# Optimization experiments

Hardware: AMD Instinct MI355X
Metric: run time of the kernel (lower is better)

The kernel has to match this reference:

```python
import jax, jax.numpy as jnp
import numpy as np

DELTA_PULL = 0.5
DELTA_PUSH = 1.5
EPS = 1e-6


def setup_inputs() -> dict:
    key = jax.random.key(0)
    k1, k2 = jax.random.split(key)
    B, C, H, W, K = 4, 16, 512, 512, 16
    embedding_maps = jax.random.normal(k1, (B, C, H, W), dtype=jnp.float32)
    instance_masks = jax.random.randint(k2, (B, K, H, W), 0, 2, dtype=jnp.int32)
    return {"embedding_maps": embedding_maps, "instance_masks": instance_masks}


def reference(embedding_maps, instance_masks):
    emb = embedding_maps                      # [B, C, H, W]
    m = (instance_masks > 0).astype(emb.dtype)  # [B, K, H, W]
    K = m.shape[1]

    # per-instance masked segment reductions over all H*W pixels
    counts = m.sum((-1, -2))                                   # [B, K]
    sums = jnp.einsum('bchw,bkhw->bkc', emb, m)                # [B, K, C]
    sq_sums = jnp.einsum('bchw,bkhw->bkc', emb * emb, m)       # [B, K, C]

    valid = counts > 0                                          # [B, K]
    safe_counts = jnp.maximum(counts, 1.0)
    means = sums / safe_counts[..., None]                       # [B, K, C] exact fg mean

    # sum over fg pixels of ||e - mean||^2 = sq_sum - 2*mean.sum + n*mean^2
    pull_k = (sq_sums - 2.0 * means * sums + counts[..., None] * means * means).sum(-1)
    pull_k = jnp.where(valid, pull_k / (counts + EPS), 0.0)     # [B, K]

    M = valid.sum(-1).astype(emb.dtype)                         # [B] num valid instances
    pull_b = pull_k.sum(-1) / jnp.maximum(M, 1.0)               # [B]

    # pairwise push between valid instance means (i < j)
    diff = means[:, :, None, :] - means[:, None, :, :]          # [B, K, K, C]
    dist = jnp.sqrt((diff * diff).sum(-1) + 1e-12)              # [B, K, K]
    iu = jnp.arange(K)
    pair = valid[:, :, None] & valid[:, None, :] & (iu[:, None] < iu[None, :])
    push_terms = jnp.where(pair, jnp.maximum(DELTA_PUSH - dist, 0.0) ** 2, 0.0)
    npairs = M * (M - 1.0) / 2.0
    push_b = jnp.where(M > 1.0, push_terms.sum((-1, -2)) / jnp.maximum(npairs, 1.0), 0.0)

    return (DELTA_PULL * pull_b + push_b).mean()
```

## Files before the change

kernel.cpp:

```cpp
#include <hip/hip_runtime.h>

#define BB 4
#define CC 16
#define KK 16
#define HWP (512 * 512)
#define TPB 1024
#define TPW 256
#define NTILES (HWP / TPB)
#define THREADS 256
#define NGROUP (TPW / 32)
#define NSLICE 16
#define WSTOT (64 + 1024 + 1024)

typedef short bf16x8 __attribute__((ext_vector_type(8)));
typedef float f32x4 __attribute__((ext_vector_type(4)));

__device__ __forceinline__ float fmaxf_(float a, float b) { return a > b ? a : b; }

__device__ __forceinline__ unsigned short f2bf(float f) {
    unsigned u = __float_as_uint(f);
    u += 0x7FFFu + ((u >> 16) & 1u);
    return (unsigned short)(u >> 16);
}
__device__ __forceinline__ unsigned pkbf(float x, float y) {
    return (unsigned)f2bf(x) | ((unsigned)f2bf(y) << 16);
}

__global__ __launch_bounds__(THREADS) void disc_mfma_kernel(
    const float* __restrict__ emb, const int* __restrict__ masks,
    float* __restrict__ ws)
{
    __shared__ __align__(16) unsigned short bits[TPB];
    __shared__ float redbuf[4][64][9];
    __shared__ float cnt_red[4][16];

    const int tid = threadIdx.x;
    const int lane = tid & 63;
    const int wave = tid >> 6;
    const int b = blockIdx.x / NTILES;
    const int tile = blockIdx.x % NTILES;
    const size_t base_px = (size_t)tile * TPB + wave * TPW;

    const int quad = lane >> 4;
    const int r = lane & 15;

    const int* mbase = masks + (size_t)b * KK * HWP + base_px + 4 * lane;
    unsigned v0 = 0, v1 = 0, v2 = 0, v3 = 0;
    #pragma unroll
    for (int k = 0; k < KK; ++k) {
        int4 mm = *(const int4*)(mbase + (size_t)k * HWP);
        v0 |= (mm.x > 0 ? 1u : 0u) << k;
        v1 |= (mm.y > 0 ? 1u : 0u) << k;
        v2 |= (mm.z > 0 ? 1u : 0u) << k;
        v3 |= (mm.w > 0 ? 1u : 0u) << k;
    }
    uint2 pk;
    pk.x = v0 | (v1 << 16);
    pk.y = v2 | (v3 << 16);
    ((uint2*)bits)[(wave * TPW) / 4 + lane] = pk;

    union { bf16x8 v; unsigned short s[8]; } Bones;
    #pragma unroll
    for (int i = 0; i < 8; ++i) Bones.s[i] = 0x3F80;

    const float* ebase = emb + ((size_t)b * CC + r) * HWP + base_px;

    f32x4 acc_s = {0.f, 0.f, 0.f, 0.f};
    f32x4 acc_q = {0.f, 0.f, 0.f, 0.f};
    f32x4 acc_c = {0.f, 0.f, 0.f, 0.f};

    #pragma unroll
    for (int g = 0; g < NGROUP; ++g) {
        const int p0 = wave * TPW + g * 32;

        uint4 bw = *(const uint4*)&bits[p0 + quad * 8];
        union { bf16x8 v; unsigned u[4]; } A;
        A.u[0] = ((bw.x >> r) & 0x00010001u) * 0x3F80u;
        A.u[1] = ((bw.y >> r) & 0x00010001u) * 0x3F80u;
        A.u[2] = ((bw.z >> r) & 0x00010001u) * 0x3F80u;
        A.u[3] = ((bw.w >> r) & 0x00010001u) * 0x3F80u;

        const float4* ep = (const float4*)(ebase + g * 32 + quad * 8);
        float4 f0 = ep[0], f1 = ep[1];
        union { bf16x8 v; unsigned u[4]; } Bf, B2;
        Bf.u[0] = pkbf(f0.x, f0.y);
        Bf.u[1] = pkbf(f0.z, f0.w);
        Bf.u[2] = pkbf(f1.x, f1.y);
        Bf.u[3] = pkbf(f1.z, f1.w);
        B2.u[0] = pkbf(f0.x * f0.x, f0.y * f0.y);
        B2.u[1] = pkbf(f0.z * f0.z, f0.w * f0.w);
        B2.u[2] = pkbf(f1.x * f1.x, f1.y * f1.y);
        B2.u[3] = pkbf(f1.z * f1.z, f1.w * f1.w);

        acc_s = __builtin_amdgcn_mfma_f32_16x16x32_bf16(A.v, Bf.v, acc_s, 0, 0, 0);
        acc_q = __builtin_amdgcn_mfma_f32_16x16x32_bf16(A.v, B2.v, acc_q, 0, 0, 0);
        acc_c = __builtin_amdgcn_mfma_f32_16x16x32_bf16(A.v, Bones.v, acc_c, 0, 0, 0);
    }

    #pragma unroll
    for (int j = 0; j < 4; ++j) {
        redbuf[wave][lane][j] = acc_s[j];
        redbuf[wave][lane][4 + j] = acc_q[j];
    }
    if (r == 0) {
        #pragma unroll
        for (int reg = 0; reg < 4; ++reg) cnt_red[wave][quad * 4 + reg] = acc_c[reg];
    }
    __syncthreads();

    float* slice = ws + (size_t)(blockIdx.x & (NSLICE - 1)) * WSTOT;
    #pragma unroll
    for (int t = 0; t < 2; ++t) {
        const int fi = tid + t * THREADS;
        const int l2 = fi >> 3, j = fi & 7;
        float v = redbuf[0][l2][j] + redbuf[1][l2][j]
                + redbuf[2][l2][j] + redbuf[3][l2][j];
        const int reg = j & 3, isq = j >> 2;
        const int krow = (l2 >> 4) * 4 + reg;
        const int ccol = l2 & 15;
        atomicAdd(&slice[64 + isq * 1024 + ((size_t)b * KK + krow) * CC + ccol], v);
    }
    if (tid < KK) {
        float ctot = cnt_red[0][tid] + cnt_red[1][tid] + cnt_red[2][tid] + cnt_red[3][tid];
        atomicAdd(&slice[b * KK + tid], ctot);
    }
}

__global__ __launch_bounds__(256) void disc_finalize_kernel(
    const float* __restrict__ ws, float* __restrict__ out)
{
    __shared__ float red[WSTOT];
    __shared__ float means[BB][KK][CC];
    __shared__ float partial[BB];
    const int tid = threadIdx.x;

    for (int idx = tid; idx < WSTOT; idx += 256) {
        float t = 0.f;
        #pragma unroll
        for (int s = 0; s < NSLICE; ++s) t += ws[(size_t)s * WSTOT + idx];
        red[idx] = t;
    }
    __syncthreads();

    const float* red_cnt = red;
    const float* red_sum = red + 64;
    const float* red_sq  = red + 64 + 1024;

    const int b = tid >> 6;
    const int lane = tid & 63;

    const float DELTA_PULL = 0.5f;
    const float DELTA_PUSH = 1.5f;
    const float EPS = 1e-6f;

    float cntk = 0.f;
    bool valid = false;
    float pull_k = 0.f;
    if (lane < KK) {
        int k = lane;
        cntk = red_cnt[b * KK + k];
        valid = cntk > 0.f;
        float safe = fmaxf_(cntk, 1.f);
        float acc_sq = 0.f, acc_ss = 0.f;
        #pragma unroll
        for (int c = 0; c < CC; ++c) {
            float sv = red_sum[(b * KK + k) * CC + c];
            means[b][k][c] = sv / safe;
            acc_sq += red_sq[(b * KK + k) * CC + c];
            acc_ss += sv * sv;
        }
        if (valid) pull_k = (acc_sq - acc_ss / cntk) / (cntk + EPS);
    }

    unsigned long long bal = __ballot(lane < KK && valid);
    float M = (float)__popcll(bal);

    float ps = pull_k;
    #pragma unroll
    for (int d = 32; d >= 1; d >>= 1) ps += __shfl_xor(ps, d, 64);
    float pull_b = ps / fmaxf_(M, 1.f);

    __syncthreads();

    float push = 0.f;
    for (int t = lane; t < KK * KK; t += 64) {
        int i = t >> 4, j = t & 15;
        if (i < j && ((bal >> i) & 1ull) && ((bal >> j) & 1ull)) {
            float d2 = 1e-12f;
            #pragma unroll
            for (int c = 0; c < CC; ++c) {
                float df = means[b][i][c] - means[b][j][c];
                d2 = fmaf(df, df, d2);
            }
            float dist = sqrtf(d2);
            float h = fmaxf_(DELTA_PUSH - dist, 0.f);
            push += h * h;
        }
    }
    #pragma unroll
    for (int d = 32; d >= 1; d >>= 1) push += __shfl_xor(push, d, 64);

    if (lane == 0) {
        float npairs = M * (M - 1.f) * 0.5f;
        float push_b = (M > 1.f) ? push / fmaxf_(npairs, 1.f) : 0.f;
        partial[b] = DELTA_PULL * pull_b + push_b;
    }
    __syncthreads();
    if (tid == 0) {
        out[0] = (partial[0] + partial[1] + partial[2] + partial[3]) * 0.25f;
    }
}

extern "C" void kernel_launch(void* const* d_in, const int* in_sizes, int n_in,
                              void* d_out, int out_size, void* d_ws, size_t ws_size,
                              hipStream_t stream) {
    const float* emb = (const float*)d_in[0];
    const int* masks = (const int*)d_in[1];
    float* ws = (float*)d_ws;

    hipMemsetAsync(d_ws, 0, NSLICE * WSTOT * sizeof(float), stream);

    dim3 grid(BB * NTILES);
    disc_mfma_kernel<<<grid, THREADS, 0, stream>>>(emb, masks, ws);
    disc_finalize_kernel<<<1, 256, 0, stream>>>(ws, (float*)d_out);
}
```

Baseline: 155.4 us.

## Stage embedding tile into LDS via global_load_lds before MFMA loop

Measured after the change: 157.2 us. About the same (+1.2%).

```diff
diff --git a/kernel.cpp b/kernel.cpp
--- a/kernel.cpp
+++ b/kernel.cpp
@@ -11,6 +11,7 @@
 #define NGROUP (TPW / 32)
 #define NSLICE 16
 #define WSTOT (64 + 1024 + 1024)
+#define ESTRIDE 1028
 
 typedef short bf16x8 __attribute__((ext_vector_type(8)));
 typedef float f32x4 __attribute__((ext_vector_type(4)));
@@ -26,10 +27,23 @@
     return (unsigned)f2bf(x) | ((unsigned)f2bf(y) << 16);
 }
 
+__device__ __forceinline__ void dma16(const float* g, float* l) {
+#if __has_builtin(__builtin_amdgcn_global_load_lds)
+    __builtin_amdgcn_global_load_lds(
+        (const __attribute__((address_space(1))) void*)g,
+        (__attribute__((address_space(3))) void*)l,
+        16, 0, 0);
+#else
+    float4 v = *(const float4*)g;
+    *(float4*)((char*)l + 16 * (threadIdx.x & 63)) = v;
+#endif
+}
+
 __global__ __launch_bounds__(THREADS) void disc_mfma_kernel(
     const float* __restrict__ emb, const int* __restrict__ masks,
     float* __restrict__ ws)
 {
+    __shared__ __align__(16) float lds_emb[CC * ESTRIDE];
     __shared__ __align__(16) unsigned short bits[TPB];
     __shared__ float redbuf[4][64][9];
     __shared__ float cnt_red[4][16];
@@ -39,12 +53,25 @@
     const int wave = tid >> 6;
     const int b = blockIdx.x / NTILES;
     const int tile = blockIdx.x % NTILES;
-    const size_t base_px = (size_t)tile * TPB + wave * TPW;
+    const size_t tile0 = (size_t)tile * TPB;
 
     const int quad = lane >> 4;
     const int r = lane & 15;
 
-    const int* mbase = masks + (size_t)b * KK * HWP + base_px + 4 * lane;
+    {
+        const float* gch = emb + ((size_t)b * CC + wave * 4) * HWP + tile0;
+        #pragma unroll
+        for (int i = 0; i < 4; ++i) {
+            const int ch = wave * 4 + i;
+            #pragma unroll
+            for (int j = 0; j < 4; ++j) {
+                dma16(gch + (size_t)i * HWP + j * 256 + lane * 4,
+                      &lds_emb[ch * ESTRIDE + j * 256]);
+            }
+        }
+    }
+
+    const int* mbase = masks + (size_t)b * KK * HWP + tile0 + wave * TPW + 4 * lane;
     unsigned v0 = 0, v1 = 0, v2 = 0, v3 = 0;
     #pragma unroll
     for (int k = 0; k < KK; ++k) {
@@ -59,11 +86,11 @@
     pk.y = v2 | (v3 << 16);
     ((uint2*)bits)[(wave * TPW) / 4 + lane] = pk;
 
+    __syncthreads();
+
     union { bf16x8 v; unsigned short s[8]; } Bones;
     #pragma unroll
     for (int i = 0; i < 8; ++i) Bones.s[i] = 0x3F80;
-
-    const float* ebase = emb + ((size_t)b * CC + r) * HWP + base_px;
 
     f32x4 acc_s = {0.f, 0.f, 0.f, 0.f};
     f32x4 acc_q = {0.f, 0.f, 0.f, 0.f};
@@ -80,8 +107,9 @@
         A.u[2] = ((bw.z >> r) & 0x00010001u) * 0x3F80u;
         A.u[3] = ((bw.w >> r) & 0x00010001u) * 0x3F80u;
 
-        const float4* ep = (const float4*)(ebase + g * 32 + quad * 8);
-        float4 f0 = ep[0], f1 = ep[1];
+        const float* ep = &lds_emb[r * ESTRIDE + p0 + quad * 8];
+        float4 f0 = *(const float4*)ep;
+        float4 f1 = *(const float4*)(ep + 4);
         union { bf16x8 v; unsigned u[4]; } Bf, B2;
         Bf.u[0] = pkbf(f0.x, f0.y);
         Bf.u[1] = pkbf(f0.z, f0.w);
```
